# Performance work log

Measured on AMD Instinct MI355X. Metric: run time of the kernel, lower is better.

The kernel has to match this reference:

```python
import jax, jax.numpy as jnp
import numpy as np

DEGREE = 7

def setup_inputs() -> dict:
    key = jax.random.key(0)
    k1, k2 = jax.random.split(key)
    input_dims, output_dims = 1024, 1024
    x = jax.random.normal(k1, (8192, input_dims), dtype=jnp.float32)
    std = 1.0 / (input_dims * (DEGREE + 1))
    lucas_coeffs = std * jax.random.normal(k2, (input_dims, output_dims, DEGREE + 1), dtype=jnp.float32)
    return {"x": x, "lucas_coeffs": lucas_coeffs}

def reference(x, lucas_coeffs):
    input_dims = lucas_coeffs.shape[0]
    x = x.reshape(-1, input_dims)
    x = jnp.tanh(x)
    # Lucas polynomial recurrence: L0=2, L1=x, L_i = x*L_{i-1} + L_{i-2}
    basis = [jnp.full_like(x, 2.0)]
    if DEGREE > 0:
        basis.append(x)
    for i in range(2, DEGREE + 1):
        basis.append(x * basis[-1] + basis[-2])
    lucas = jnp.stack(basis, axis=-1)  # [b, i, d]
    y = jnp.einsum('bid,iod->bo', lucas, lucas_coeffs)
    return y
```

## Files before the change

kernel.cpp:

```cpp
#include <hip/hip_runtime.h>
#include <hip/hip_bf16.h>


typedef __attribute__((ext_vector_type(8)))  short  short8;
typedef __attribute__((ext_vector_type(4)))  unsigned short ushort4v;
typedef __attribute__((ext_vector_type(8)))  unsigned short ushort8;
typedef __attribute__((ext_vector_type(4)))  float  float4v;
typedef __attribute__((ext_vector_type(4)))  unsigned int uint4v;

#define M_DIM 8192
#define I_DIM 1024
#define O_DIM 1024
#define K_DIM 8192
#define BM 128
#define BN 128
#define BK 64
#define KSPLIT 2
#define KHALF (K_DIM / KSPLIT)
#define NSTEP (KHALF / BK)

__device__ __forceinline__ unsigned short f2bf(float f) {
    unsigned int u = __float_as_uint(f);
    u += 0x7FFFu + ((u >> 16) & 1u);
    return (unsigned short)(u >> 16);
}

__global__ __launch_bounds__(256) void prep_zt_kernel(const float* __restrict__ x,
                                                      unsigned short* __restrict__ T,
                                                      float* __restrict__ outz) {
    const int nthr = gridDim.x * 256;
    const int gid  = blockIdx.x * 256 + threadIdx.x;

    const int zN = (M_DIM * O_DIM) / 4;
    const float4v z = {0.f, 0.f, 0.f, 0.f};
    for (int i = gid; i < zN; i += nthr)
        *(float4v*)(outz + (size_t)i * 4) = z;

    const int tN = (M_DIM * I_DIM) / 8;
    for (int i = gid; i < tN; i += nthr) {
        const size_t idx = (size_t)i * 8;
        float4v v0 = *(const float4v*)(x + idx);
        float4v v1 = *(const float4v*)(x + idx + 4);
        unsigned short t[8];
        t[0] = f2bf(tanhf(v0[0])); t[1] = f2bf(tanhf(v0[1]));
        t[2] = f2bf(tanhf(v0[2])); t[3] = f2bf(tanhf(v0[3]));
        t[4] = f2bf(tanhf(v1[0])); t[5] = f2bf(tanhf(v1[1]));
        t[6] = f2bf(tanhf(v1[2])); t[7] = f2bf(tanhf(v1[3]));
        ushort8 o;
        #pragma unroll
        for (int p = 0; p < 4; ++p) { o[2 * p] = t[p]; o[2 * p + 1] = t[p + 4]; }
        *(ushort8*)(T + idx) = o;
    }
}

__global__ __launch_bounds__(256) void prep_tr_kernel(const float* __restrict__ c,
                                                      unsigned short* __restrict__ Bt) {
    __shared__ unsigned short S[32][64 * 8 + 8];
    const int tid = threadIdx.x;
    const int tb  = blockIdx.x;
    const int i0 = (tb >> 5) * 64;
    const int o0 = (tb & 31) * 32;
    #pragma unroll 4
    for (int p = 0; p < 16; ++p) {
        const int il = p * 4 + (tid >> 6);
        const int e  = (tid & 63) * 4;
        const float* src = c + (size_t)(i0 + il) * 8192 + o0 * 8 + e;
        float4v v = *(const float4v*)src;
        ushort4v u;
        u[0] = f2bf(v[0]); u[1] = f2bf(v[1]); u[2] = f2bf(v[2]); u[3] = f2bf(v[3]);
        *(ushort4v*)&S[e >> 3][il * 8 + (e & 7)] = u;
    }
    __syncthreads();
    #pragma unroll 4
    for (int q = 0; q < 16; ++q) {
        const int ol = q * 2 + (tid >> 7);
        const int ch = (tid & 127) * 4;
        ushort4v u = *(const ushort4v*)&S[ol][ch];
        *(ushort4v*)(Bt + (size_t)(o0 + ol) * K_DIM + i0 * 8 + ch) = u;
    }
}

__device__ __forceinline__ short8 lucas_frag(unsigned int tb) {
    const float t = __uint_as_float(tb << 16);
    const float L2v = fmaf(t, t, 2.0f);
    const float L3v = fmaf(t, L2v, t);
    const float L4v = fmaf(t, L3v, L2v);
    const float L5v = fmaf(t, L4v, L3v);
    const float L6v = fmaf(t, L5v, L4v);
    const float L7v = fmaf(t, L6v, L5v);
    union { uint4v u; short8 s; } r;
#if __has_builtin(__builtin_amdgcn_cvt_pk_bf16_f32)
    {
        auto p0 = __builtin_amdgcn_cvt_pk_bf16_f32(2.0f, t);
        auto p1 = __builtin_amdgcn_cvt_pk_bf16_f32(L2v, L3v);
        auto p2 = __builtin_amdgcn_cvt_pk_bf16_f32(L4v, L5v);
        auto p3 = __builtin_amdgcn_cvt_pk_bf16_f32(L6v, L7v);
        __builtin_memcpy(&r.u[0], &p0, 4);
        __builtin_memcpy(&r.u[1], &p1, 4);
        __builtin_memcpy(&r.u[2], &p2, 4);
        __builtin_memcpy(&r.u[3], &p3, 4);
    }
#else
    {
        r.u[0] = 0x4000u | (tb << 16);
        r.u[1] = __builtin_amdgcn_perm(__float_as_uint(L3v), __float_as_uint(L2v), 0x07060302);
        r.u[2] = __builtin_amdgcn_perm(__float_as_uint(L5v), __float_as_uint(L4v), 0x07060302);
        r.u[3] = __builtin_amdgcn_perm(__float_as_uint(L7v), __float_as_uint(L6v), 0x07060302);
    }
#endif
    return r.s;
}

__global__ __launch_bounds__(256, 2) void gemm_kernel(const unsigned short* __restrict__ T,
                                                      const unsigned short* __restrict__ Bt,
                                                      float* __restrict__ out) {
    __shared__ unsigned short Bs[4][BN * BK];
    __shared__ unsigned short Ts[4][BM * 8];

    const int tid  = threadIdx.x;
    const int lane = tid & 63;
    const int wave = tid >> 6;
    const int n0 = blockIdx.x * BN;
    const int m0 = blockIdx.y * BM;
    const int k0 = blockIdx.z * KHALF;

    const int wm0  = wave * 32;
    const int l16  = lane & 15;
    const int quad = lane >> 4;

    const int srow   = lane >> 3;
    const int il     = lane & 7;
    const int gchunk = il ^ srow;

    float4v acc[2][8];
    const float4v zero = {0.f, 0.f, 0.f, 0.f};
    #pragma unroll
    for (int a = 0; a < 2; ++a)
        #pragma unroll
        for (int b = 0; b < 8; ++b) acc[a][b] = zero;

    auto stage = [&](int buf, int kt) {
        #pragma unroll
        for (int r = 0; r < 4; ++r) {
            const int rowb = r * 32 + wave * 8;
            const unsigned short* gB = Bt + (size_t)(n0 + rowb + srow) * K_DIM + kt + gchunk * 8;
            __builtin_amdgcn_global_load_lds(
                (const __attribute__((address_space(1))) unsigned int*)gB,
                (__attribute__((address_space(3))) unsigned int*)&Bs[buf][rowb * BK], 16, 0, 0);
        }
        if (wave < 2) {
            const unsigned short* gT = T + (size_t)(m0 + wave * 64 + lane) * I_DIM + kt / 8;
            __builtin_amdgcn_global_load_lds(
                (const __attribute__((address_space(1))) unsigned int*)gT,
                (__attribute__((address_space(3))) unsigned int*)&Ts[buf][wave * 64 * 8], 16, 0, 0);
        }
    };

    auto compute = [&](int cur) {
        unsigned int tw[2];
        #pragma unroll
        for (int tt = 0; tt < 2; ++tt)
            tw[tt] = *(const unsigned int*)&Ts[cur][(wm0 + tt * 16 + l16) * 8 + quad * 2];

        #pragma unroll
        for (int k2 = 0; k2 < 2; ++k2) {
            short8 af[2];
            af[0] = lucas_frag(k2 ? (tw[0] >> 16) : (tw[0] & 0xffffu));
            af[1] = lucas_frag(k2 ? (tw[1] >> 16) : (tw[1] & 0xffffu));
            #pragma unroll
            for (int g = 0; g < 2; ++g) {
                short8 bfr[4];
                #pragma unroll
                for (int j = 0; j < 4; ++j) {
                    const int brow = (g * 4 + j) * 16 + l16;
                    bfr[j] = *(const short8*)&Bs[cur][brow * BK + (((k2 * 4 + quad) ^ (l16 & 7)) * 8)];
                }
                #pragma unroll
                for (int tt = 0; tt < 2; ++tt)
                    #pragma unroll
                    for (int j = 0; j < 4; ++j)
                        acc[tt][g * 4 + j] = __builtin_amdgcn_mfma_f32_16x16x32_bf16(
                            af[tt], bfr[j], acc[tt][g * 4 + j], 0, 0, 0);
            }
        }
    };

    stage(0, k0);
    stage(1, k0 + BK);

    for (int s = 0; s < NSTEP - 2; ++s) {
        stage((s + 2) & 3, k0 + (s + 2) * BK);
        if (wave < 2) asm volatile("s_waitcnt vmcnt(10)" ::: "memory");
        else          asm volatile("s_waitcnt vmcnt(8)"  ::: "memory");
        __builtin_amdgcn_s_barrier();
        compute(s & 3);
    }
    if (wave < 2) asm volatile("s_waitcnt vmcnt(5)" ::: "memory");
    else          asm volatile("s_waitcnt vmcnt(4)" ::: "memory");
    __builtin_amdgcn_s_barrier();
    compute((NSTEP - 2) & 3);
    asm volatile("s_waitcnt vmcnt(0)" ::: "memory");
    __builtin_amdgcn_s_barrier();
    compute((NSTEP - 1) & 3);

    #pragma unroll
    for (int tt = 0; tt < 2; ++tt) {
        #pragma unroll
        for (int tn = 0; tn < 8; ++tn) {
            const int col = n0 + tn * 16 + l16;
            #pragma unroll
            for (int r = 0; r < 4; ++r) {
                const int row = m0 + wm0 + tt * 16 + quad * 4 + r;
                atomicAdd(&out[(size_t)row * O_DIM + col], acc[tt][tn][r]);
            }
        }
    }
}

__global__ __launch_bounds__(256) void naive_kernel(const float* __restrict__ x,
                                                    const float* __restrict__ c,
                                                    float* __restrict__ out) {
    int idx = blockIdx.x * 256 + threadIdx.x;
    int b = idx >> 10;
    int o = idx & 1023;
    const float* xb = x + (size_t)b * I_DIM;
    float acc = 0.f;
    for (int i = 0; i < I_DIM; ++i) {
        float t = tanhf(xb[i]);
        float L[8];
        L[0] = 2.0f; L[1] = t;
        #pragma unroll
        for (int d = 2; d < 8; ++d) L[d] = t * L[d - 1] + L[d - 2];
        const float* cc = c + (size_t)i * 8192 + o * 8;
        #pragma unroll
        for (int d = 0; d < 8; ++d) acc += L[d] * cc[d];
    }
    out[idx] = acc;
}

extern "C" void kernel_launch(void* const* d_in, const int* in_sizes, int n_in,
                              void* d_out, int out_size, void* d_ws, size_t ws_size,
                              hipStream_t stream) {
    const float* x      = (const float*)d_in[0];
    const float* coeffs = (const float*)d_in[1];
    float* out = (float*)d_out;

    const size_t btBytes = (size_t)O_DIM * K_DIM * sizeof(unsigned short);
    const size_t tBytes  = (size_t)M_DIM * I_DIM * sizeof(unsigned short);

    if (ws_size >= btBytes + tBytes) {
        unsigned short* Bt = (unsigned short*)d_ws;
        unsigned short* T  = (unsigned short*)((char*)d_ws + btBytes);

        const int xBlocks = (I_DIM / 64) * (I_DIM / 32);
        prep_tr_kernel<<<xBlocks, 256, 0, stream>>>(coeffs, Bt);
        prep_zt_kernel<<<2048, 256, 0, stream>>>(x, T, out);

        dim3 grid(O_DIM / BN, M_DIM / BM, KSPLIT);
        gemm_kernel<<<grid, 256, 0, stream>>>(T, Bt, out);
    } else {
        naive_kernel<<<(M_DIM * O_DIM) / 256, 256, 0, stream>>>(x, coeffs, out);
    }
}
```

Baseline: 254.2 us.

## Enlarge GEMM tile to 256x256 with 8 waves and interleaved prefetch

Doubles the block tile to 256x256 and uses 512 threads (8 waves arranged as 2x4), so each wave computes a 128x64 sub-tile. The prefetch of the next stage is split into parts and interleaved with the MFMA phases. Extra barriers and s_setprio are added around the MFMA bursts. This raises data reuse per loaded byte and reduces global traffic, at the cost of larger LDS use, more registers, fewer blocks in the grid (256) and more barriers per step.

```diff
diff --git a/kernel.cpp b/kernel.cpp
--- a/kernel.cpp
+++ b/kernel.cpp
@@ -12,8 +12,8 @@
 #define I_DIM 1024
 #define O_DIM 1024
 #define K_DIM 8192
-#define BM 128
-#define BN 128
+#define BM 256
+#define BN 256
 #define BK 64
 #define KSPLIT 2
 #define KHALF (K_DIM / KSPLIT)
@@ -111,7 +111,7 @@
     return r.s;
 }
 
-__global__ __launch_bounds__(256, 2) void gemm_kernel(const unsigned short* __restrict__ T,
+__global__ __launch_bounds__(512, 2) void gemm_kernel(const unsigned short* __restrict__ T,
                                                       const unsigned short* __restrict__ Bt,
                                                       float* __restrict__ out) {
     __shared__ unsigned short Bs[4][BN * BK];
@@ -120,11 +120,12 @@
     const int tid  = threadIdx.x;
     const int lane = tid & 63;
     const int wave = tid >> 6;
+    const int wm = wave >> 2;
+    const int wn = wave & 3;
     const int n0 = blockIdx.x * BN;
     const int m0 = blockIdx.y * BM;
     const int k0 = blockIdx.z * KHALF;
 
-    const int wm0  = wave * 32;
     const int l16  = lane & 15;
     const int quad = lane >> 4;
 
@@ -132,23 +133,25 @@
     const int il     = lane & 7;
     const int gchunk = il ^ srow;
 
-    float4v acc[2][8];
+    float4v acc[8][4];
     const float4v zero = {0.f, 0.f, 0.f, 0.f};
     #pragma unroll
-    for (int a = 0; a < 2; ++a)
-        #pragma unroll
-        for (int b = 0; b < 8; ++b) acc[a][b] = zero;
-
-    auto stage = [&](int buf, int kt) {
-        #pragma unroll
-        for (int r = 0; r < 4; ++r) {
-            const int rowb = r * 32 + wave * 8;
+    for (int a = 0; a < 8; ++a)
+        #pragma unroll
+        for (int b = 0; b < 4; ++b) acc[a][b] = zero;
+
+    auto stageB = [&](int buf, int kt, int part) {
+        #pragma unroll
+        for (int r = part * 2; r < part * 2 + 2; ++r) {
+            const int rowb = wave * 32 + r * 8;
             const unsigned short* gB = Bt + (size_t)(n0 + rowb + srow) * K_DIM + kt + gchunk * 8;
             __builtin_amdgcn_global_load_lds(
                 (const __attribute__((address_space(1))) unsigned int*)gB,
                 (__attribute__((address_space(3))) unsigned int*)&Bs[buf][rowb * BK], 16, 0, 0);
         }
-        if (wave < 2) {
+    };
+    auto stageT = [&](int buf, int kt) {
+        if (wave < 4) {
             const unsigned short* gT = T + (size_t)(m0 + wave * 64 + lane) * I_DIM + kt / 8;
             __builtin_amdgcn_global_load_lds(
                 (const __attribute__((address_space(1))) unsigned int*)gT,
@@ -156,62 +159,71 @@
         }
     };
 
-    auto compute = [&](int cur) {
-        unsigned int tw[2];
-        #pragma unroll
-        for (int tt = 0; tt < 2; ++tt)
-            tw[tt] = *(const unsigned int*)&Ts[cur][(wm0 + tt * 16 + l16) * 8 + quad * 2];
-
-        #pragma unroll
-        for (int k2 = 0; k2 < 2; ++k2) {
-            short8 af[2];
-            af[0] = lucas_frag(k2 ? (tw[0] >> 16) : (tw[0] & 0xffffu));
-            af[1] = lucas_frag(k2 ? (tw[1] >> 16) : (tw[1] & 0xffffu));
+    stageB(0, k0, 0); stageB(0, k0, 1); stageT(0, k0);
+    stageB(1, k0 + BK, 0); stageB(1, k0 + BK, 1); stageT(1, k0 + BK);
+
+    for (int s = 0; s < NSTEP; ++s) {
+        const int cur  = s & 3;
+        const int pre  = (s + 2) & 3;
+        const int kpre = k0 + (s + 2) * BK;
+        const bool do_pre = (s + 2 < NSTEP);
+
+        if (s + 1 < NSTEP) {
+            if (wave < 4) asm volatile("s_waitcnt vmcnt(5)" ::: "memory");
+            else          asm volatile("s_waitcnt vmcnt(4)" ::: "memory");
+        } else {
+            asm volatile("s_waitcnt vmcnt(0)" ::: "memory");
+        }
+        __builtin_amdgcn_s_barrier();
+
+        short8 bfr[4];
+        #pragma unroll
+        for (int p = 0; p < 4; ++p) {
+            const int k2 = p >> 1;
+            const int mh = p & 1;
+            if (mh == 0) {
+                #pragma unroll
+                for (int nt = 0; nt < 4; ++nt) {
+                    const int brow = wn * 64 + nt * 16 + l16;
+                    bfr[nt] = *(const short8*)
+                        &Bs[cur][brow * BK + (((k2 * 4 + quad) ^ (l16 & 7)) * 8)];
+                }
+            }
+            unsigned int tw[4];
             #pragma unroll
-            for (int g = 0; g < 2; ++g) {
-                short8 bfr[4];
+            for (int mt = 0; mt < 4; ++mt) {
+                const int mrow = wm * 128 + mh * 64 + mt * 16 + l16;
+                tw[mt] = *(const unsigned int*)&Ts[cur][mrow * 8 + quad * 2];
+            }
+            if (do_pre) {
+                if (p == 0)      stageB(pre, kpre, 0);
+                else if (p == 1) stageB(pre, kpre, 1);
+                else if (p == 2) stageT(pre, kpre);
+            }
+            __builtin_amdgcn_s_barrier();
+            __builtin_amdgcn_s_setprio(1);
+            #pragma unroll
+            for (int mt = 0; mt < 4; ++mt) {
+                const short8 af = lucas_frag(k2 ? (tw[mt] >> 16) : (tw[mt] & 0xffffu));
                 #pragma unroll
-                for (int j = 0; j < 4; ++j) {
-                    const int brow = (g * 4 + j) * 16 + l16;
-                    bfr[j] = *(const short8*)&Bs[cur][brow * BK + (((k2 * 4 + quad) ^ (l16 & 7)) * 8)];
-                }
-                #pragma unroll
-                for (int tt = 0; tt < 2; ++tt)
-                    #pragma unroll
-                    for (int j = 0; j < 4; ++j)
-                        acc[tt][g * 4 + j] = __builtin_amdgcn_mfma_f32_16x16x32_bf16(
-                            af[tt], bfr[j], acc[tt][g * 4 + j], 0, 0, 0);
-            }
-        }
-    };
-
-    stage(0, k0);
-    stage(1, k0 + BK);
-
-    for (int s = 0; s < NSTEP - 2; ++s) {
-        stage((s + 2) & 3, k0 + (s + 2) * BK);
-        if (wave < 2) asm volatile("s_waitcnt vmcnt(10)" ::: "memory");
-        else          asm volatile("s_waitcnt vmcnt(8)"  ::: "memory");
-        __builtin_amdgcn_s_barrier();
-        compute(s & 3);
-    }
-    if (wave < 2) asm volatile("s_waitcnt vmcnt(5)" ::: "memory");
-    else          asm volatile("s_waitcnt vmcnt(4)" ::: "memory");
-    __builtin_amdgcn_s_barrier();
-    compute((NSTEP - 2) & 3);
-    asm volatile("s_waitcnt vmcnt(0)" ::: "memory");
-    __builtin_amdgcn_s_barrier();
-    compute((NSTEP - 1) & 3);
+                for (int nt = 0; nt < 4; ++nt)
+                    acc[mh * 4 + mt][nt] = __builtin_amdgcn_mfma_f32_16x16x32_bf16(
+                        af, bfr[nt], acc[mh * 4 + mt][nt], 0, 0, 0);
+            }
+            __builtin_amdgcn_s_setprio(0);
+            __builtin_amdgcn_s_barrier();
+        }
+    }
 
     #pragma unroll
-    for (int tt = 0; tt < 2; ++tt) {
-        #pragma unroll
-        for (int tn = 0; tn < 8; ++tn) {
-            const int col = n0 + tn * 16 + l16;
+    for (int i = 0; i < 8; ++i) {
+        #pragma unroll
+        for (int nt = 0; nt < 4; ++nt) {
+            const int col = n0 + wn * 64 + nt * 16 + l16;
             #pragma unroll
             for (int r = 0; r < 4; ++r) {
-                const int row = m0 + wm0 + tt * 16 + quad * 4 + r;
-                atomicAdd(&out[(size_t)row * O_DIM + col], acc[tt][tn][r]);
+                const int row = m0 + wm * 128 + (i >> 2) * 64 + (i & 3) * 16 + quad * 4 + r;
+                atomicAdd(&out[(size_t)row * O_DIM + col], acc[i][nt][r]);
             }
         }
     }
@@ -257,7 +269,7 @@
         prep_zt_kernel<<<2048, 256, 0, stream>>>(x, T, out);
 
         dim3 grid(O_DIM / BN, M_DIM / BM, KSPLIT);
-        gemm_kernel<<<grid, 256, 0, stream>>>(T, Bt, out);
+        gemm_kernel<<<grid, 512, 0, stream>>>(T, Bt, out);
     } else {
         naive_kernel<<<(M_DIM * O_DIM) / 256, 256, 0, stream>>>(x, coeffs, out);
     }
```

After: 281.9 us. +10.9%, slower.
